# Kernel optimization log

Measured on AMD Instinct MI355X. Metric: run time of the kernel, lower is better.

The kernel has to match this reference:

```python
import jax, jax.numpy as jnp
import numpy as np

HEADS = 4
DIM_HEAD = 32
SCALE = DIM_HEAD ** -0.5


def setup_inputs() -> dict:
    key = jax.random.key(0)
    k1, k2, k3 = jax.random.split(key, 3)
    dim = 128
    hidden = HEADS * DIM_HEAD  # 128
    x = jax.random.normal(k1, (4, dim, 64, 64), dtype=jnp.float32)
    w_qkv = jax.random.normal(k2, (3 * hidden, dim), dtype=jnp.float32) * (dim ** -0.5)
    w_out = jax.random.normal(k3, (dim, hidden), dtype=jnp.float32) * (hidden ** -0.5)
    b_out = jnp.zeros((dim,), dtype=jnp.float32)
    return {"x": x, "w_qkv": w_qkv, "w_out": w_out, "b_out": b_out}


def reference(x, w_qkv, w_out, b_out):
    b, c, h, w = x.shape
    n = h * w
    # 1x1 conv == channel matmul per pixel
    qkv = jnp.einsum('oc,bchw->bohw', w_qkv, x)  # [b, 3*hidden, h, w]
    q, k, v = jnp.split(qkv, 3, axis=1)
    # b (heads d) x y -> b heads d (x y)
    def to_heads(t):
        return t.reshape(b, HEADS, DIM_HEAD, n)
    q = to_heads(q) * SCALE
    k = to_heads(k)
    v = to_heads(v)
    sim = jnp.einsum('bhdi,bhdj->bhij', q, k)          # [b, heads, n, n]
    attn = jax.nn.softmax(sim, axis=-1)
    out = jnp.einsum('bhij,bhdj->bhid', attn, v)        # [b, heads, n, d]
    # b h (x y) d -> b (h d) x y
    out = out.transpose(0, 1, 3, 2).reshape(b, HEADS * DIM_HEAD, h, w)
    out = jnp.einsum('oc,bchw->bohw', w_out, out) + b_out[None, :, None, None]
    return out
```

## Files before the change

kernel.cpp:

```cpp
#include <hip/hip_runtime.h>
#include <math.h>

#define NHEAD 4
#define DHEAD 32
#define NPIX  4096
#define CIN   128

typedef __bf16 bf16_t;
typedef __bf16 bf16x8 __attribute__((ext_vector_type(8)));
typedef __bf16 bf16x4 __attribute__((ext_vector_type(4)));
typedef float  f32x4  __attribute__((ext_vector_type(4)));

constexpr float QSCALE = 0.17677669529663687f * 1.4426950408889634f;

__global__ void __launch_bounds__(256) prep_weights(
    const float* __restrict__ w_qkv, const float* __restrict__ w_out,
    ushort* __restrict__ wqkv_bf, ushort* __restrict__ wout_bf) {
  const int i4 = (blockIdx.x * 256 + threadIdx.x) * 4;
  const float* src;
  ushort* dst;
  float sc = 1.f;
  if (i4 < 49152) {
    src = w_qkv + i4; dst = wqkv_bf + i4;
    if (i4 < 16384) sc = QSCALE;
  } else {
    src = w_out + (i4 - 49152); dst = wout_bf + (i4 - 49152);
  }
  float4 v = *(const float4*)src;
  bf16x4 o = {(bf16_t)(v.x * sc), (bf16_t)(v.y * sc),
              (bf16_t)(v.z * sc), (bf16_t)(v.w * sc)};
  *(bf16x4*)dst = o;
}

__global__ void __launch_bounds__(384) qkv_mfma(
    const float* __restrict__ x, const ushort* __restrict__ wqkv,
    ushort* __restrict__ qb, ushort* __restrict__ kb, ushort* __restrict__ vT) {
  __shared__ ushort Xls[32 * 136];
  const int tid = threadIdx.x, cg = tid >> 6, lane = tid & 63;
  const int n = lane & 15, quad = lane >> 4;
  const int b = blockIdx.y, p0 = blockIdx.x * 32;

  bf16x8 wf[4][4];
#pragma unroll
  for (int t1 = 0; t1 < 4; ++t1)
#pragma unroll
    for (int k = 0; k < 4; ++k)
      wf[t1][k] = *(const bf16x8*)(wqkv +
          (size_t)(cg * 64 + t1 * 16 + n) * CIN + k * 32 + quad * 8);

  if (tid < 256) {
    const int pc = tid & 7;
    const int c  = (tid >> 3) * 4;
    const float* xp = x + ((size_t)b * CIN + c) * NPIX + p0 + pc * 4;
    float4 r0 = *(const float4*)xp;
    float4 r1 = *(const float4*)(xp + NPIX);
    float4 r2 = *(const float4*)(xp + 2 * NPIX);
    float4 r3 = *(const float4*)(xp + 3 * NPIX);
    bf16x4 w0 = {(bf16_t)r0.x, (bf16_t)r1.x, (bf16_t)r2.x, (bf16_t)r3.x};
    bf16x4 w1 = {(bf16_t)r0.y, (bf16_t)r1.y, (bf16_t)r2.y, (bf16_t)r3.y};
    bf16x4 w2 = {(bf16_t)r0.z, (bf16_t)r1.z, (bf16_t)r2.z, (bf16_t)r3.z};
    bf16x4 w3 = {(bf16_t)r0.w, (bf16_t)r1.w, (bf16_t)r2.w, (bf16_t)r3.w};
    *(bf16x4*)&Xls[(pc * 4 + 0) * 136 + c] = w0;
    *(bf16x4*)&Xls[(pc * 4 + 1) * 136 + c] = w1;
    *(bf16x4*)&Xls[(pc * 4 + 2) * 136 + c] = w2;
    *(bf16x4*)&Xls[(pc * 4 + 3) * 136 + c] = w3;
  }
  __syncthreads();

  f32x4 acc[4][2];
#pragma unroll
  for (int i = 0; i < 4; ++i)
#pragma unroll
    for (int j = 0; j < 2; ++j) acc[i][j] = (f32x4){0.f, 0.f, 0.f, 0.f};

  const bool isv = (cg >= 4);
#pragma unroll
  for (int k = 0; k < 4; ++k) {
    bf16x8 xf[2];
#pragma unroll
    for (int pt = 0; pt < 2; ++pt)
      xf[pt] = *(const bf16x8*)&Xls[(pt * 16 + n) * 136 + k * 32 + quad * 8];
    if (!isv) {
#pragma unroll
      for (int wt = 0; wt < 4; ++wt)
#pragma unroll
        for (int pt = 0; pt < 2; ++pt)
          acc[wt][pt] = __builtin_amdgcn_mfma_f32_16x16x32_bf16(
              wf[wt][k], xf[pt], acc[wt][pt], 0, 0, 0);
    } else {
#pragma unroll
      for (int ct = 0; ct < 4; ++ct)
#pragma unroll
        for (int pt = 0; pt < 2; ++pt)
          acc[ct][pt] = __builtin_amdgcn_mfma_f32_16x16x32_bf16(
              xf[pt], wf[ct][k], acc[ct][pt], 0, 0, 0);
    }
  }

  if (!isv) {
    ushort* dst0 = (cg < 2) ? qb : kb;
#pragma unroll
    for (int wt = 0; wt < 4; ++wt) {
      const int ch = (cg & 1) * 64 + wt * 16 + quad * 4;
      const int head = ch >> 5, d = ch & 31;
#pragma unroll
      for (int pt = 0; pt < 2; ++pt) {
        const int p = p0 + pt * 16 + n;
        f32x4 a = acc[wt][pt];
        bf16x4 o = {(bf16_t)a[0], (bf16_t)a[1], (bf16_t)a[2], (bf16_t)a[3]};
        *(bf16x4*)(dst0 + ((size_t)(b * NHEAD + head) * NPIX + p) * DHEAD + d) = o;
      }
    }
  } else {
#pragma unroll
    for (int ct = 0; ct < 4; ++ct) {
      const int ch = (cg & 1) * 64 + ct * 16 + n;
      const int head = ch >> 5, d = ch & 31;
#pragma unroll
      for (int pt = 0; pt < 2; ++pt) {
        const int p = p0 + pt * 16 + quad * 4;
        f32x4 a = acc[ct][pt];
        bf16x4 o = {(bf16_t)a[0], (bf16_t)a[1], (bf16_t)a[2], (bf16_t)a[3]};
        *(bf16x4*)(vT + ((size_t)(b * NHEAD + head) * DHEAD + d) * NPIX + p) = o;
      }
    }
  }
}

__device__ __forceinline__ void ft_load(const ushort* kb0, const ushort* vb0,
                                        int t, bf16x8* kf, bf16x8* vf) {
#pragma unroll
  for (int p = 0; p < 2; ++p) {
#pragma unroll
    for (int s = 0; s < 2; ++s)
      kf[p * 2 + s] = *(const bf16x8*)(kb0 + (size_t)(t * 64 + p * 32 + s * 4) * DHEAD);
#pragma unroll
    for (int dp = 0; dp < 2; ++dp)
      vf[p * 2 + dp] = *(const bf16x8*)(vb0 + (size_t)dp * 16 * NPIX + t * 64 + p * 32);
  }
}

__device__ __forceinline__ void ft_compute(const bf16x8* qf, const bf16x8* kf,
                                           const bf16x8* vf, const bf16x8 ones,
                                           f32x4 O[8][2], f32x4* Ol) {
  const f32x4 zero = {0.f, 0.f, 0.f, 0.f};
#pragma unroll
  for (int p = 0; p < 2; ++p) {
#pragma unroll
    for (int rp = 0; rp < 8; ++rp) {
      f32x4 sa = __builtin_amdgcn_mfma_f32_16x16x32_bf16(kf[p * 2 + 0], qf[rp], zero, 0, 0, 0);
      f32x4 sb = __builtin_amdgcn_mfma_f32_16x16x32_bf16(kf[p * 2 + 1], qf[rp], zero, 0, 0, 0);
      bf16x8 pf;
#pragma unroll
      for (int r = 0; r < 4; ++r) {
        pf[r]     = (bf16_t)__builtin_amdgcn_exp2f(sa[r]);
        pf[r + 4] = (bf16_t)__builtin_amdgcn_exp2f(sb[r]);
      }
      O[rp][0] = __builtin_amdgcn_mfma_f32_16x16x32_bf16(pf, vf[p * 2 + 0], O[rp][0], 0, 0, 0);
      O[rp][1] = __builtin_amdgcn_mfma_f32_16x16x32_bf16(pf, vf[p * 2 + 1], O[rp][1], 0, 0, 0);
      Ol[rp]   = __builtin_amdgcn_mfma_f32_16x16x32_bf16(pf, ones, Ol[rp], 0, 0, 0);
    }
  }
}

__global__ void __launch_bounds__(256, 2) flash_mfma(
    const ushort* __restrict__ qb, const ushort* __restrict__ kbuf,
    const ushort* __restrict__ vTb, float* __restrict__ part) {
  const int tid = threadIdx.x, wave = tid >> 6, lane = tid & 63;
  const int n = lane & 15, quad = lane >> 4;
  const int js = blockIdx.y, bh = blockIdx.z;
  const int qrel = blockIdx.x * 512 + wave * 128;

  const ushort* kg = kbuf + (size_t)bh * NPIX * DHEAD;
  const ushort* vg = vTb + (size_t)bh * DHEAD * NPIX;

  bf16x8 qf[8];
#pragma unroll
  for (int rp = 0; rp < 8; ++rp)
    qf[rp] = *(const bf16x8*)(qb +
        ((size_t)bh * NPIX + qrel + rp * 16 + n) * DHEAD + quad * 8);

  f32x4 O[8][2], Ol[8];
#pragma unroll
  for (int rp = 0; rp < 8; ++rp) {
    O[rp][0] = (f32x4){0.f, 0.f, 0.f, 0.f};
    O[rp][1] = (f32x4){0.f, 0.f, 0.f, 0.f};
    Ol[rp]   = (f32x4){0.f, 0.f, 0.f, 0.f};
  }
  const bf16_t one = (bf16_t)1.0f;
  const bf16x8 ones = {one, one, one, one, one, one, one, one};

  const int pk = ((n >> 2) << 3) | (n & 3);
  const ushort* kb0 = kg + (size_t)(js * 1024 + pk) * DHEAD + quad * 8;
  const ushort* vb0 = vg + (size_t)n * NPIX + js * 1024 + quad * 8;

  bf16x8 kA[4], vA[4], kB[4], vB[4];
  ft_load(kb0, vb0, 0, kA, vA);
#pragma unroll 1
  for (int t = 0; t < 16; t += 2) {
    ft_load(kb0, vb0, t + 1, kB, vB);
    ft_compute(qf, kA, vA, ones, O, Ol);
    if (t + 2 < 16) ft_load(kb0, vb0, t + 2, kA, vA);
    ft_compute(qf, kB, vB, ones, O, Ol);
  }

  float* pb = part + ((size_t)js * 65536 + (size_t)bh * NPIX + qrel) * 36;
#pragma unroll
  for (int rp = 0; rp < 8; ++rp)
#pragma unroll
    for (int r = 0; r < 4; ++r) {
      const int q = rp * 16 + quad * 4 + r;
      pb[(size_t)q * 36 + n]      = O[rp][0][r];
      pb[(size_t)q * 36 + 16 + n] = O[rp][1][r];
      if (n == 0) pb[(size_t)q * 36 + 32] = Ol[rp][r];
    }
}

__global__ void __launch_bounds__(256) combine4(
    const float* __restrict__ part, ushort* __restrict__ aoT) {
  const int idx = blockIdx.x * 256 + threadIdx.x;
  const float* p0 = part + (size_t)idx * 36;
  const float* p1 = p0 + (size_t)65536 * 36;
  const float* p2 = p1 + (size_t)65536 * 36;
  const float* p3 = p2 + (size_t)65536 * 36;
  const float inv = 1.f / (p0[32] + p1[32] + p2[32] + p3[32]);
#pragma unroll
  for (int t = 0; t < 4; ++t) {
    float4 a0 = ((const float4*)p0)[2 * t], a1 = ((const float4*)p0)[2 * t + 1];
    float4 b0 = ((const float4*)p1)[2 * t], b1 = ((const float4*)p1)[2 * t + 1];
    float4 c0 = ((const float4*)p2)[2 * t], c1 = ((const float4*)p2)[2 * t + 1];
    float4 d0 = ((const float4*)p3)[2 * t], d1 = ((const float4*)p3)[2 * t + 1];
    bf16x8 o = {(bf16_t)((a0.x + b0.x + c0.x + d0.x) * inv),
                (bf16_t)((a0.y + b0.y + c0.y + d0.y) * inv),
                (bf16_t)((a0.z + b0.z + c0.z + d0.z) * inv),
                (bf16_t)((a0.w + b0.w + c0.w + d0.w) * inv),
                (bf16_t)((a1.x + b1.x + c1.x + d1.x) * inv),
                (bf16_t)((a1.y + b1.y + c1.y + d1.y) * inv),
                (bf16_t)((a1.z + b1.z + c1.z + d1.z) * inv),
                (bf16_t)((a1.w + b1.w + c1.w + d1.w) * inv)};
    *(bf16x8*)(aoT + (size_t)idx * 32 + t * 8) = o;
  }
}

__global__ void __launch_bounds__(512) out_mfma(
    const ushort* __restrict__ aoT, const ushort* __restrict__ wob,
    const float* __restrict__ bias, float* __restrict__ out) {
  const int tid = threadIdx.x, wv = tid >> 6, lane = tid & 63;
  const int n = lane & 15, quad = lane >> 4;
  const int b = blockIdx.y;
  const int oc0 = (wv & 1) * 64;
  const int p = blockIdx.x * 64 + (wv >> 1) * 16 + n;

  bf16x8 wf[4][4];
#pragma unroll
  for (int mt = 0; mt < 4; ++mt)
#pragma unroll
    for (int k = 0; k < 4; ++k)
      wf[mt][k] = *(const bf16x8*)(wob + (size_t)(oc0 + mt * 16 + n) * CIN + k * 32 + quad * 8);

  bf16x8 bfr[4];
#pragma unroll
  for (int k = 0; k < 4; ++k)
    bfr[k] = *(const bf16x8*)(aoT + ((size_t)(b * NHEAD + k) * NPIX + p) * DHEAD + quad * 8);

  f32x4 acc[4];
#pragma unroll
  for (int mt = 0; mt < 4; ++mt) acc[mt] = (f32x4){0.f, 0.f, 0.f, 0.f};
#pragma unroll
  for (int k = 0; k < 4; ++k)
#pragma unroll
    for (int mt = 0; mt < 4; ++mt)
      acc[mt] = __builtin_amdgcn_mfma_f32_16x16x32_bf16(wf[mt][k], bfr[k], acc[mt], 0, 0, 0);

#pragma unroll
  for (int mt = 0; mt < 4; ++mt) {
    const int oc = oc0 + mt * 16 + quad * 4;
#pragma unroll
    for (int r = 0; r < 4; ++r)
      out[((size_t)b * CIN + oc + r) * NPIX + p] = acc[mt][r] + bias[oc + r];
  }
}

extern "C" void kernel_launch(void* const* d_in, const int* in_sizes, int n_in,
                              void* d_out, int out_size, void* d_ws, size_t ws_size,
                              hipStream_t stream) {
  const float* x     = (const float*)d_in[0];
  const float* w_qkv = (const float*)d_in[1];
  const float* w_out = (const float*)d_in[2];
  const float* b_out = (const float*)d_in[3];
  float* out = (float*)d_out;

  char* base = (char*)d_ws;
  ushort* qb      = (ushort*)base;
  ushort* kb      = (ushort*)(base + (size_t)4 * 1024 * 1024);
  ushort* vT      = (ushort*)(base + (size_t)8 * 1024 * 1024);
  ushort* aoT     = (ushort*)(base + (size_t)12 * 1024 * 1024);
  ushort* wqkv_bf = (ushort*)(base + (size_t)16 * 1024 * 1024);
  ushort* wout_bf = (ushort*)(base + (size_t)16 * 1024 * 1024 + 96 * 1024);
  float*  part    = (float*)(base + (size_t)17 * 1024 * 1024);

  prep_weights<<<dim3(64), 256, 0, stream>>>(w_qkv, w_out, wqkv_bf, wout_bf);
  qkv_mfma<<<dim3(128, 4), 384, 0, stream>>>(x, wqkv_bf, qb, kb, vT);
  flash_mfma<<<dim3(8, 4, 16), 256, 0, stream>>>(qb, kb, vT, part);
  combine4<<<dim3(256), 256, 0, stream>>>(part, aoT);
  out_mfma<<<dim3(64, 4), 512, 0, stream>>>(aoT, wout_bf, b_out, out);
}
```

Before: 140.4 us.

## Stage K/V tiles in LDS with double buffering and pre-swizzle weight fragments

The flash kernel now cooperatively loads 128-key K and V tiles into double-buffered shared memory and reads MFMA fragments from there, instead of each wave fetching its own copy from global memory. Each wave now handles 64 queries rather than 128, the grid is a flat 1024 blocks with head-interleaved ordering, and the occupancy hint rises to 4 blocks. Weights are pre-swizzled into a per-lane fragment layout so the qkv and out-projection kernels do contiguous fragment loads, and the out-projection kernel moves to 256-thread blocks. The risks are extra LDS traffic and barrier stalls per tile, and fewer queries per wave to amortise each K/V fragment.

```diff
diff --git a/kernel.cpp b/kernel.cpp
--- a/kernel.cpp
+++ b/kernel.cpp
@@ -5,6 +5,7 @@
 #define DHEAD 32
 #define NPIX  4096
 #define CIN   128
+#define KTILE 128
 
 typedef __bf16 bf16_t;
 typedef __bf16 bf16x8 __attribute__((ext_vector_type(8)));
@@ -13,27 +14,35 @@
 
 constexpr float QSCALE = 0.17677669529663687f * 1.4426950408889634f;
 
-__global__ void __launch_bounds__(256) prep_weights(
-    const float* __restrict__ w_qkv, const float* __restrict__ w_out,
-    ushort* __restrict__ wqkv_bf, ushort* __restrict__ wout_bf) {
-  const int i4 = (blockIdx.x * 256 + threadIdx.x) * 4;
-  const float* src;
-  ushort* dst;
-  float sc = 1.f;
-  if (i4 < 49152) {
-    src = w_qkv + i4; dst = wqkv_bf + i4;
-    if (i4 < 16384) sc = QSCALE;
+__global__ void __launch_bounds__(256) prep_swz(
+    const float* __restrict__ wqkv, const float* __restrict__ wout,
+    ushort* __restrict__ wq_s, ushort* __restrict__ wo_s) {
+  const int gid = blockIdx.x * 256 + threadIdx.x;
+  if (gid < 6144) {
+    const int lane = gid & 63, n = lane & 15, quad = lane >> 4;
+    const int fragid = gid >> 6;
+    const int cg = fragid >> 4, t1 = (fragid >> 2) & 3, k = fragid & 3;
+    const float sc = (cg < 2) ? QSCALE : 1.f;
+    const float* src = wqkv + (size_t)(cg * 64 + t1 * 16 + n) * CIN + k * 32 + quad * 8;
+    bf16x8 o;
+#pragma unroll
+    for (int e = 0; e < 8; ++e) o[e] = (bf16_t)(src[e] * sc);
+    *(bf16x8*)(wq_s + (size_t)gid * 8) = o;
   } else {
-    src = w_out + (i4 - 49152); dst = wout_bf + (i4 - 49152);
-  }
-  float4 v = *(const float4*)src;
-  bf16x4 o = {(bf16_t)(v.x * sc), (bf16_t)(v.y * sc),
-              (bf16_t)(v.z * sc), (bf16_t)(v.w * sc)};
-  *(bf16x4*)dst = o;
+    const int oid = gid - 6144;
+    const int lane = oid & 63, n = lane & 15, quad = lane >> 4;
+    const int fragid = oid >> 6;
+    const int h = fragid >> 4, mt = (fragid >> 2) & 3, k = fragid & 3;
+    const float* src = wout + (size_t)(h * 64 + mt * 16 + n) * CIN + k * 32 + quad * 8;
+    bf16x8 o;
+#pragma unroll
+    for (int e = 0; e < 8; ++e) o[e] = (bf16_t)src[e];
+    *(bf16x8*)(wo_s + (size_t)oid * 8) = o;
+  }
 }
 
 __global__ void __launch_bounds__(384) qkv_mfma(
-    const float* __restrict__ x, const ushort* __restrict__ wqkv,
+    const float* __restrict__ x, const ushort* __restrict__ wswz,
     ushort* __restrict__ qb, ushort* __restrict__ kb, ushort* __restrict__ vT) {
   __shared__ ushort Xls[32 * 136];
   const int tid = threadIdx.x, cg = tid >> 6, lane = tid & 63;
@@ -41,12 +50,14 @@
   const int b = blockIdx.y, p0 = blockIdx.x * 32;
 
   bf16x8 wf[4][4];
-#pragma unroll
-  for (int t1 = 0; t1 < 4; ++t1)
-#pragma unroll
-    for (int k = 0; k < 4; ++k)
-      wf[t1][k] = *(const bf16x8*)(wqkv +
-          (size_t)(cg * 64 + t1 * 16 + n) * CIN + k * 32 + quad * 8);
+  {
+    const ushort* wbase = wswz + (size_t)cg * 8192;
+#pragma unroll
+    for (int t1 = 0; t1 < 4; ++t1)
+#pragma unroll
+      for (int k = 0; k < 4; ++k)
+        wf[t1][k] = *(const bf16x8*)(wbase + ((t1 * 4 + k) * 64 + lane) * 8);
+  }
 
   if (tid < 256) {
     const int pc = tid & 7;
@@ -127,92 +138,121 @@
   }
 }
 
-__device__ __forceinline__ void ft_load(const ushort* kb0, const ushort* vb0,
-                                        int t, bf16x8* kf, bf16x8* vf) {
-#pragma unroll
-  for (int p = 0; p < 2; ++p) {
-#pragma unroll
-    for (int s = 0; s < 2; ++s)
-      kf[p * 2 + s] = *(const bf16x8*)(kb0 + (size_t)(t * 64 + p * 32 + s * 4) * DHEAD);
-#pragma unroll
-    for (int dp = 0; dp < 2; ++dp)
-      vf[p * 2 + dp] = *(const bf16x8*)(vb0 + (size_t)dp * 16 * NPIX + t * 64 + p * 32);
-  }
-}
-
-__device__ __forceinline__ void ft_compute(const bf16x8* qf, const bf16x8* kf,
-                                           const bf16x8* vf, const bf16x8 ones,
-                                           f32x4 O[8][2], f32x4* Ol) {
-  const f32x4 zero = {0.f, 0.f, 0.f, 0.f};
-#pragma unroll
-  for (int p = 0; p < 2; ++p) {
-#pragma unroll
-    for (int rp = 0; rp < 8; ++rp) {
-      f32x4 sa = __builtin_amdgcn_mfma_f32_16x16x32_bf16(kf[p * 2 + 0], qf[rp], zero, 0, 0, 0);
-      f32x4 sb = __builtin_amdgcn_mfma_f32_16x16x32_bf16(kf[p * 2 + 1], qf[rp], zero, 0, 0, 0);
-      bf16x8 pf;
-#pragma unroll
-      for (int r = 0; r < 4; ++r) {
-        pf[r]     = (bf16_t)__builtin_amdgcn_exp2f(sa[r]);
-        pf[r + 4] = (bf16_t)__builtin_amdgcn_exp2f(sb[r]);
-      }
-      O[rp][0] = __builtin_amdgcn_mfma_f32_16x16x32_bf16(pf, vf[p * 2 + 0], O[rp][0], 0, 0, 0);
-      O[rp][1] = __builtin_amdgcn_mfma_f32_16x16x32_bf16(pf, vf[p * 2 + 1], O[rp][1], 0, 0, 0);
-      Ol[rp]   = __builtin_amdgcn_mfma_f32_16x16x32_bf16(pf, ones, Ol[rp], 0, 0, 0);
-    }
-  }
-}
-
-__global__ void __launch_bounds__(256, 2) flash_mfma(
+__global__ void __launch_bounds__(256, 4) flash_mfma(
     const ushort* __restrict__ qb, const ushort* __restrict__ kbuf,
     const ushort* __restrict__ vTb, float* __restrict__ part) {
+  __shared__ ushort Kls[2][KTILE * 32];
+  __shared__ ushort Vls[2][32 * 136];
+
   const int tid = threadIdx.x, wave = tid >> 6, lane = tid & 63;
   const int n = lane & 15, quad = lane >> 4;
-  const int js = blockIdx.y, bh = blockIdx.z;
-  const int qrel = blockIdx.x * 512 + wave * 128;
-
-  const ushort* kg = kbuf + (size_t)bh * NPIX * DHEAD;
-  const ushort* vg = vTb + (size_t)bh * DHEAD * NPIX;
-
-  bf16x8 qf[8];
-#pragma unroll
-  for (int rp = 0; rp < 8; ++rp)
+  const int id = blockIdx.x;
+  const int bh = (id & 7) * 2 + ((id >> 3) & 1);
+  const int r  = id >> 4;
+  const int qt = r & 15;
+  const int ks = r >> 4;
+  const int q0 = qt * 256 + wave * 64;
+  const int k0 = ks * 1024;
+
+  const ushort* kg = kbuf + (size_t)bh * NPIX * DHEAD + (size_t)k0 * DHEAD;
+  const ushort* vg = vTb + (size_t)bh * DHEAD * NPIX + k0;
+
+  bf16x8 qf[4];
+#pragma unroll
+  for (int rp = 0; rp < 4; ++rp)
     qf[rp] = *(const bf16x8*)(qb +
-        ((size_t)bh * NPIX + qrel + rp * 16 + n) * DHEAD + quad * 8);
-
-  f32x4 O[8][2], Ol[8];
-#pragma unroll
-  for (int rp = 0; rp < 8; ++rp) {
+        ((size_t)bh * NPIX + q0 + rp * 16 + n) * DHEAD + quad * 8);
+
+  f32x4 O[4][2], Ol[4];
+#pragma unroll
+  for (int rp = 0; rp < 4; ++rp) {
     O[rp][0] = (f32x4){0.f, 0.f, 0.f, 0.f};
     O[rp][1] = (f32x4){0.f, 0.f, 0.f, 0.f};
     Ol[rp]   = (f32x4){0.f, 0.f, 0.f, 0.f};
   }
   const bf16_t one = (bf16_t)1.0f;
   const bf16x8 ones = {one, one, one, one, one, one, one, one};
-
+  const f32x4 zero = {0.f, 0.f, 0.f, 0.f};
+
+  const int skey = tid >> 2, sseg = tid & 3;
+  const int sd   = tid >> 4, svs  = tid & 15;
   const int pk = ((n >> 2) << 3) | (n & 3);
-  const ushort* kb0 = kg + (size_t)(js * 1024 + pk) * DHEAD + quad * 8;
-  const ushort* vb0 = vg + (size_t)n * NPIX + js * 1024 + quad * 8;
-
-  bf16x8 kA[4], vA[4], kB[4], vB[4];
-  ft_load(kb0, vb0, 0, kA, vA);
+
+  bf16x8 kv0, kv1, vv0, vv1;
+  kv0 = *(const bf16x8*)(kg + (size_t)skey * DHEAD + sseg * 8);
+  kv1 = *(const bf16x8*)(kg + (size_t)(skey + 64) * DHEAD + sseg * 8);
+  vv0 = *(const bf16x8*)(vg + (size_t)sd * NPIX + svs * 8);
+  vv1 = *(const bf16x8*)(vg + (size_t)(sd + 16) * NPIX + svs * 8);
+  *(bf16x8*)&Kls[0][skey * 32 + sseg * 8]       = kv0;
+  *(bf16x8*)&Kls[0][(skey + 64) * 32 + sseg * 8] = kv1;
+  *(bf16x8*)&Vls[0][sd * 136 + svs * 8]          = vv0;
+  *(bf16x8*)&Vls[0][(sd + 16) * 136 + svs * 8]   = vv1;
+  __syncthreads();
+
 #pragma unroll 1
-  for (int t = 0; t < 16; t += 2) {
-    ft_load(kb0, vb0, t + 1, kB, vB);
-    ft_compute(qf, kA, vA, ones, O, Ol);
-    if (t + 2 < 16) ft_load(kb0, vb0, t + 2, kA, vA);
-    ft_compute(qf, kB, vB, ones, O, Ol);
-  }
-
-  float* pb = part + ((size_t)js * 65536 + (size_t)bh * NPIX + qrel) * 36;
-#pragma unroll
-  for (int rp = 0; rp < 8; ++rp)
-#pragma unroll
-    for (int r = 0; r < 4; ++r) {
-      const int q = rp * 16 + quad * 4 + r;
-      pb[(size_t)q * 36 + n]      = O[rp][0][r];
-      pb[(size_t)q * 36 + 16 + n] = O[rp][1][r];
-      if (n == 0) pb[(size_t)q * 36 + 32] = Ol[rp][r];
+  for (int tile = 0; tile < 8; ++tile) {
+    const int cur = tile & 1;
+    if (tile < 7) {
+      const ushort* kgt = kg + (size_t)(tile + 1) * KTILE * DHEAD;
+      const ushort* vgt = vg + (tile + 1) * KTILE;
+      kv0 = *(const bf16x8*)(kgt + (size_t)skey * DHEAD + sseg * 8);
+      kv1 = *(const bf16x8*)(kgt + (size_t)(skey + 64) * DHEAD + sseg * 8);
+      vv0 = *(const bf16x8*)(vgt + (size_t)sd * NPIX + svs * 8);
+      vv1 = *(const bf16x8*)(vgt + (size_t)(sd + 16) * NPIX + svs * 8);
+    }
+
+#pragma unroll
+    for (int sub = 0; sub < 4; ++sub) {
+      const ushort* Kb = &Kls[cur][sub * 32 * 32];
+      const bf16x8 f0 = *(const bf16x8*)&Kb[pk * 32 + quad * 8];
+      const bf16x8 f1 = *(const bf16x8*)&Kb[(pk + 4) * 32 + quad * 8];
+      const bf16x8 f2 = *(const bf16x8*)&Vls[cur][n * 136 + sub * 32 + quad * 8];
+      const bf16x8 f3 = *(const bf16x8*)&Vls[cur][(n + 16) * 136 + sub * 32 + quad * 8];
+#pragma unroll
+      for (int hp = 0; hp < 2; ++hp) {
+        f32x4 s[2][2];
+#pragma unroll
+        for (int j = 0; j < 2; ++j) {
+          s[j][0] = __builtin_amdgcn_mfma_f32_16x16x32_bf16(f0, qf[hp * 2 + j], zero, 0, 0, 0);
+          s[j][1] = __builtin_amdgcn_mfma_f32_16x16x32_bf16(f1, qf[hp * 2 + j], zero, 0, 0, 0);
+        }
+        bf16x8 pf[2];
+#pragma unroll
+        for (int j = 0; j < 2; ++j)
+#pragma unroll
+          for (int rr = 0; rr < 4; ++rr) {
+            pf[j][rr]     = (bf16_t)__builtin_amdgcn_exp2f(s[j][0][rr]);
+            pf[j][rr + 4] = (bf16_t)__builtin_amdgcn_exp2f(s[j][1][rr]);
+          }
+#pragma unroll
+        for (int j = 0; j < 2; ++j) {
+          const int rp = hp * 2 + j;
+          O[rp][0] = __builtin_amdgcn_mfma_f32_16x16x32_bf16(pf[j], f2, O[rp][0], 0, 0, 0);
+          O[rp][1] = __builtin_amdgcn_mfma_f32_16x16x32_bf16(pf[j], f3, O[rp][1], 0, 0, 0);
+          Ol[rp]   = __builtin_amdgcn_mfma_f32_16x16x32_bf16(pf[j], ones, Ol[rp], 0, 0, 0);
+        }
+      }
+    }
+
+    if (tile < 7) {
+      const int nb = cur ^ 1;
+      *(bf16x8*)&Kls[nb][skey * 32 + sseg * 8]        = kv0;
+      *(bf16x8*)&Kls[nb][(skey + 64) * 32 + sseg * 8] = kv1;
+      *(bf16x8*)&Vls[nb][sd * 136 + svs * 8]          = vv0;
+      *(bf16x8*)&Vls[nb][(sd + 16) * 136 + svs * 8]   = vv1;
+    }
+    __syncthreads();
+  }
+
+  float* pb = part + ((size_t)ks * 65536 + (size_t)bh * NPIX + q0) * 36;
+#pragma unroll
+  for (int rp = 0; rp < 4; ++rp)
+#pragma unroll
+    for (int rr = 0; rr < 4; ++rr) {
+      const int q = rp * 16 + quad * 4 + rr;
+      pb[(size_t)q * 36 + n]      = O[rp][0][rr];
+      pb[(size_t)q * 36 + 16 + n] = O[rp][1][rr];
+      if (n == 0) pb[(size_t)q * 36 + 32] = Ol[rp][rr];
     }
 }
 
@@ -242,21 +282,25 @@
   }
 }
 
-__global__ void __launch_bounds__(512) out_mfma(
-    const ushort* __restrict__ aoT, const ushort* __restrict__ wob,
+__global__ void __launch_bounds__(256) out_mfma(
+    const ushort* __restrict__ aoT, const ushort* __restrict__ wswz,
     const float* __restrict__ bias, float* __restrict__ out) {
   const int tid = threadIdx.x, wv = tid >> 6, lane = tid & 63;
   const int n = lane & 15, quad = lane >> 4;
   const int b = blockIdx.y;
-  const int oc0 = (wv & 1) * 64;
-  const int p = blockIdx.x * 64 + (wv >> 1) * 16 + n;
+  const int h = wv & 1;
+  const int oc0 = h * 64;
+  const int p = blockIdx.x * 32 + (wv >> 1) * 16 + n;
 
   bf16x8 wf[4][4];
-#pragma unroll
-  for (int mt = 0; mt < 4; ++mt)
-#pragma unroll
-    for (int k = 0; k < 4; ++k)
-      wf[mt][k] = *(const bf16x8*)(wob + (size_t)(oc0 + mt * 16 + n) * CIN + k * 32 + quad * 8);
+  {
+    const ushort* wbase = wswz + (size_t)h * 8192;
+#pragma unroll
+    for (int mt = 0; mt < 4; ++mt)
+#pragma unroll
+      for (int k = 0; k < 4; ++k)
+        wf[mt][k] = *(const bf16x8*)(wbase + ((mt * 4 + k) * 64 + lane) * 8);
+  }
 
   bf16x8 bfr[4];
 #pragma unroll
@@ -276,8 +320,8 @@
   for (int mt = 0; mt < 4; ++mt) {
     const int oc = oc0 + mt * 16 + quad * 4;
 #pragma unroll
-    for (int r = 0; r < 4; ++r)
-      out[((size_t)b * CIN + oc + r) * NPIX + p] = acc[mt][r] + bias[oc + r];
+    for (int rr = 0; rr < 4; ++rr)
+      out[((size_t)b * CIN + oc + rr) * NPIX + p] = acc[mt][rr] + bias[oc + rr];
   }
 }
 
@@ -291,17 +335,17 @@
   float* out = (float*)d_out;
 
   char* base = (char*)d_ws;
-  ushort* qb      = (ushort*)base;
-  ushort* kb      = (ushort*)(base + (size_t)4 * 1024 * 1024);
-  ushort* vT      = (ushort*)(base + (size_t)8 * 1024 * 1024);
-  ushort* aoT     = (ushort*)(base + (size_t)12 * 1024 * 1024);
-  ushort* wqkv_bf = (ushort*)(base + (size_t)16 * 1024 * 1024);
-  ushort* wout_bf = (ushort*)(base + (size_t)16 * 1024 * 1024 + 96 * 1024);
-  float*  part    = (float*)(base + (size_t)17 * 1024 * 1024);
-
-  prep_weights<<<dim3(64), 256, 0, stream>>>(w_qkv, w_out, wqkv_bf, wout_bf);
-  qkv_mfma<<<dim3(128, 4), 384, 0, stream>>>(x, wqkv_bf, qb, kb, vT);
-  flash_mfma<<<dim3(8, 4, 16), 256, 0, stream>>>(qb, kb, vT, part);
+  ushort* qb   = (ushort*)base;
+  ushort* kb   = (ushort*)(base + (size_t)4 * 1024 * 1024);
+  ushort* vT   = (ushort*)(base + (size_t)8 * 1024 * 1024);
+  ushort* aoT  = (ushort*)(base + (size_t)12 * 1024 * 1024);
+  ushort* wq_s = (ushort*)(base + (size_t)16 * 1024 * 1024);
+  ushort* wo_s = (ushort*)(base + (size_t)16 * 1024 * 1024 + 96 * 1024);
+  float*  part = (float*)(base + (size_t)17 * 1024 * 1024);
+
+  prep_swz<<<dim3(32), 256, 0, stream>>>(w_qkv, w_out, wq_s, wo_s);
+  qkv_mfma<<<dim3(128, 4), 384, 0, stream>>>(x, wq_s, qb, kb, vT);
+  flash_mfma<<<dim3(1024), 256, 0, stream>>>(qb, kb, vT, part);
   combine4<<<dim3(256), 256, 0, stream>>>(part, aoT);
-  out_mfma<<<dim3(64, 4), 512, 0, stream>>>(aoT, wout_bf, b_out, out);
-}
+  out_mfma<<<dim3(128, 4), 256, 0, stream>>>(aoT, wo_s, b_out, out);
+}
```

New measurement: 145.0 us. 3.2% more time.
